# Kernel optimization log

Measured on AMD Instinct MI355X. Metric: run time of the kernel, lower is better.

## Reference

```python
import jax, jax.numpy as jnp
import numpy as np

B, NQ, NC = 4, 512, 2048
DQ, DC, C = 1024, 768, 1024
H = 16
HD = C // H
L = 2
EPS = 1e-5


def _ln(x, g, b):
    m = jnp.mean(x, axis=-1, keepdims=True)
    v = jnp.mean((x - m) ** 2, axis=-1, keepdims=True)
    return (x - m) * jax.lax.rsqrt(v + EPS) * g + b


def setup_inputs() -> dict:
    key = jax.random.key(0)
    ks = iter(jax.random.split(key, 16))
    s = 0.02
    inp = {}
    inp['query'] = jax.random.normal(next(ks), (B, NQ, DQ), dtype=jnp.float32)
    inp['context'] = jax.random.normal(next(ks), (B, NC, DC), dtype=jnp.float32)
    mask = jax.random.randint(next(ks), (B, NC), 0, 2, dtype=jnp.int32)
    inp['context_mask'] = mask.at[:, 0].set(1)  # guarantee >=1 valid key per row
    inp['Wqp'] = jax.random.normal(next(ks), (DQ, C), dtype=jnp.float32) * s
    inp['bqp'] = jnp.zeros((C,), jnp.float32)
    inp['Wcp'] = jax.random.normal(next(ks), (DC, C), dtype=jnp.float32) * s
    inp['bcp'] = jnp.zeros((C,), jnp.float32)
    inp['Wq'] = jax.random.normal(next(ks), (L, C, C), dtype=jnp.float32) * s
    inp['bq'] = jnp.zeros((L, C), jnp.float32)
    inp['Wkv'] = jax.random.normal(next(ks), (L, C, 2 * C), dtype=jnp.float32) * s
    inp['bkv'] = jnp.zeros((L, 2 * C), jnp.float32)
    inp['Wo'] = jax.random.normal(next(ks), (L, C, C), dtype=jnp.float32) * s
    inp['bo'] = jnp.zeros((L, C), jnp.float32)
    inp['g1'] = jnp.ones((L, C), jnp.float32)
    inp['beta1'] = jnp.zeros((L, C), jnp.float32)
    inp['W1'] = jax.random.normal(next(ks), (L, C, 4 * C), dtype=jnp.float32) * s
    inp['bf1'] = jnp.zeros((L, 4 * C), jnp.float32)
    inp['W2'] = jax.random.normal(next(ks), (L, 4 * C, C), dtype=jnp.float32) * s
    inp['bf2'] = jnp.zeros((L, C), jnp.float32)
    inp['g2'] = jnp.ones((L, C), jnp.float32)
    inp['beta2'] = jnp.zeros((L, C), jnp.float32)
    inp['gf'] = jnp.ones((C,), jnp.float32)
    inp['betaf'] = jnp.zeros((C,), jnp.float32)
    return inp


def reference(query, context, context_mask, Wqp, bqp, Wcp, bcp, Wq, bq, Wkv, bkv,
              Wo, bo, g1, beta1, W1, bf1, W2, bf2, g2, beta2, gf, betaf):
    scale = HD ** -0.5
    q = query @ Wqp + bqp            # [B,NQ,C]
    c = context @ Wcp + bcp          # [B,NC,C]
    neg = (context_mask == 0)[:, None, None, :]  # [B,1,1,NC]
    for l in range(L):
        qn = _ln(q, g1[l], beta1[l])
        qh = (qn @ Wq[l] + bq[l]).reshape(B, NQ, H, HD).transpose(0, 2, 1, 3)
        kv = (c @ Wkv[l] + bkv[l]).reshape(B, NC, 2, H, HD).transpose(2, 0, 3, 1, 4)
        k, v = kv[0], kv[1]          # [B,H,NC,HD]
        attn = jnp.einsum('bhqd,bhkd->bhqk', qh, k) * scale
        attn = jnp.where(neg, -jnp.inf, attn)
        attn = jax.nn.softmax(attn, axis=-1)
        out = jnp.einsum('bhqk,bhkd->bhqd', attn, v)
        out = out.transpose(0, 2, 1, 3).reshape(B, NQ, C)
        q = q + (out @ Wo[l] + bo[l])
        h = _ln(q, g2[l], beta2[l])
        q = q + (jax.nn.gelu(h @ W1[l] + bf1[l], approximate=False) @ W2[l] + bf2[l])
    return _ln(q, gf, betaf)
```

## Files before the change

### kernel.cpp

```cpp
#include <hip/hip_runtime.h>
#include <hip/hip_bf16.h>
#include <math.h>

typedef __hip_bfloat16 bf16;
using short8 = __attribute__((ext_vector_type(8))) short;
using f32x4  = __attribute__((ext_vector_type(4))) float;

#define B_    4
#define NQ_   512
#define NC_   2048
#define DQ_   1024
#define DC_   768
#define C_    1024
#define H_    16
#define HD_   64
#define EPS_  1e-5f

__device__ __forceinline__ float ldin(const void* p, size_t i, int f32) {
    return f32 ? ((const float*)p)[i]
               : __bfloat162float(((const bf16*)p)[i]);
}
__device__ __forceinline__ unsigned bfb(float f) {
    return (unsigned)__builtin_bit_cast(unsigned short, __float2bfloat16(f));
}

typedef const __attribute__((address_space(1))) unsigned int ga_u32;
typedef __attribute__((address_space(3))) unsigned int ls_u32;
__device__ __forceinline__ void gl16(const void* g, void* l) {
    __builtin_amdgcn_global_load_lds((ga_u32*)g, (ls_u32*)l, 16, 0, 0);
}

__global__ __launch_bounds__(256)
void sniff_k(const void* __restrict__ q, int* __restrict__ flag)
{
    __shared__ int red[256];
    const unsigned* w = (const unsigned*)q;
    const int t = threadIdx.x;
    int cnt = 0;
    for (int i = t; i < 1024; i += 256) {
        unsigned e = (w[i] >> 7) & 0xFFu;
        cnt += (e >= 0x70u && e <= 0x82u) ? 1 : 0;
    }
    red[t] = cnt; __syncthreads();
    for (int s = 128; s > 0; s >>= 1) { if (t < s) red[t] += red[t + s]; __syncthreads(); }
    if (t == 0) flag[0] = (red[0] > 512) ? 0 : 1;
}

__global__ __launch_bounds__(256)
void cvt_k(const void* __restrict__ src, bf16* __restrict__ dst, int n8,
           const int* __restrict__ dtf)
{
    const int i = blockIdx.x * 256 + threadIdx.x;
    if (i >= n8) return;
    if (dtf[0]) {
        const float* s = (const float*)src + (size_t)i * 8;
        float4 a = *(const float4*)s, b = *(const float4*)(s + 4);
        uint4 o;
        o.x = bfb(a.x) | (bfb(a.y) << 16);
        o.y = bfb(a.z) | (bfb(a.w) << 16);
        o.z = bfb(b.x) | (bfb(b.y) << 16);
        o.w = bfb(b.z) | (bfb(b.w) << 16);
        *(uint4*)(dst + (size_t)i * 8) = o;
    } else {
        *(uint4*)(dst + (size_t)i * 8) = *(const uint4*)((const bf16*)src + (size_t)i * 8);
    }
}

struct KTr {
    const void* src[6];
    bf16*       dst[6];
    long long   off[6];
    int ld[6], K[6], N[6];
    int start[7];
    int njobs;
};

__global__ __launch_bounds__(256)
void tr_all(KTr J, const int* __restrict__ dtf)
{
    __shared__ short T[64 * 65];
    const int f32 = dtf[0];
    const int t = threadIdx.x;
    int bid = blockIdx.x, j = 0;
    while (j + 1 < J.njobs && bid >= J.start[j + 1]) ++j;
    const int tt = bid - J.start[j];
    const int nx = J.N[j] >> 6;
    const int n0 = (tt % nx) * 64, k0 = (tt / nx) * 64;
    const int ld = J.ld[j], K = J.K[j];
    {
        const int k = t >> 2, nq = (t & 3) * 16;
        size_t si = (size_t)J.off[j] + (size_t)(k0 + k) * ld + n0 + nq;
        short v[16];
        if (f32) {
            const float* s = (const float*)J.src[j] + si;
#pragma unroll
            for (int u = 0; u < 4; u++) {
                float4 f = *(const float4*)(s + u * 4);
                v[u*4+0] = (short)bfb(f.x); v[u*4+1] = (short)bfb(f.y);
                v[u*4+2] = (short)bfb(f.z); v[u*4+3] = (short)bfb(f.w);
            }
        } else {
            const bf16* s = (const bf16*)J.src[j] + si;
#pragma unroll
            for (int u = 0; u < 2; u++) {
                uint4 x = *(const uint4*)(s + u * 8);
                unsigned a[4] = {x.x, x.y, x.z, x.w};
#pragma unroll
                for (int m = 0; m < 4; m++) {
                    v[u*8 + m*2]     = (short)(a[m] & 0xffffu);
                    v[u*8 + m*2 + 1] = (short)(a[m] >> 16);
                }
            }
        }
#pragma unroll
        for (int jj = 0; jj < 16; jj++) T[k * 65 + nq + jj] = v[jj];
    }
    __syncthreads();
    {
        const int n = t >> 2, kq = (t & 3) * 16;
        unsigned pk[8];
#pragma unroll
        for (int u = 0; u < 8; u++) {
            unsigned lo = (unsigned short)T[(kq + u*2)     * 65 + n];
            unsigned hi = (unsigned short)T[(kq + u*2 + 1) * 65 + n];
            pk[u] = lo | (hi << 16);
        }
        bf16* d = J.dst[j] + (size_t)(n0 + n) * K + k0 + kq;
        *(uint4*)(d)     = make_uint4(pk[0], pk[1], pk[2], pk[3]);
        *(uint4*)(d + 8) = make_uint4(pk[4], pk[5], pk[6], pk[7]);
    }
}

template<int ACT, int ACC, int OUTF32, int BM, int BN>
__global__ __launch_bounds__(256)
void gemm_bf(const bf16* __restrict__ A, int lda,
             const bf16* __restrict__ Wt,
             const void* __restrict__ bias, size_t boff, float bscale,
             void* __restrict__ outp, int M, int N, int K,
             const int* __restrict__ dtf)
{
    __shared__ short As[2][BM * 32];
    __shared__ short Bs[2][BN * 32];
    constexpr int MI = (BM == 128 && BN == 128) ? 4 : 2;
    constexpr int NJ = (BM == 64) ? 2 : 4;
    const int t  = threadIdx.x;
    const int nwg = gridDim.x * gridDim.y;
    int flat = blockIdx.y * gridDim.x + blockIdx.x;
    flat = (flat & 7) * (nwg >> 3) + (flat >> 3);
    const int row0 = (flat / gridDim.x) * BM, col0 = (flat % gridDim.x) * BN;
    const int wv = t >> 6, l = t & 63;
    const int lm = l & 15, lq = l >> 4;
    const int lr = l >> 2, lc = l & 3;
    const int swc  = lc ^ ((lr >> 1) & 3);
    const int koff = (lq ^ ((lm >> 1) & 3)) << 3;
    const int wr = (BM == 128 && BN == 128) ? (wv >> 1) * 64
                 : (BM == 128) ? wv * 32 : (wv >> 1) * 32;
    const int wc = (BN == 128) ? (wv & 1) * 64
                 : (BM == 128) ? 0 : (wv & 1) * 32;

    const bf16* Ag0 = A + (size_t)(row0 + ((BM == 128) ? wv * 32 : wv * 16) + lr) * lda + swc * 8;
    const bf16* Ag1 = Ag0 + (size_t)16 * lda;
    const bf16* Bg0 = Wt + (size_t)(col0 + ((BN == 128) ? wv * 32 : wv * 16) + lr) * K + swc * 8;
    const bf16* Bg1 = Bg0 + (size_t)16 * K;

    f32x4 acc[MI][NJ];
#pragma unroll
    for (int i = 0; i < MI; i++)
#pragma unroll
        for (int j = 0; j < NJ; j++) { acc[i][j][0]=0.f; acc[i][j][1]=0.f; acc[i][j][2]=0.f; acc[i][j][3]=0.f; }

    auto stage = [&](int b, int k0) {
        if constexpr (BM == 128) {
            gl16(Ag0 + k0, &As[b][(wv * 32) * 32]);
            gl16(Ag1 + k0, &As[b][(wv * 32 + 16) * 32]);
        } else {
            gl16(Ag0 + k0, &As[b][(wv * 16) * 32]);
        }
        if constexpr (BN == 128) {
            gl16(Bg0 + k0, &Bs[b][(wv * 32) * 32]);
            gl16(Bg1 + k0, &Bs[b][(wv * 32 + 16) * 32]);
        } else {
            gl16(Bg0 + k0, &Bs[b][(wv * 16) * 32]);
        }
    };

    const int nt = K >> 5;
    stage(0, 0);
    __syncthreads();
    int cur = 0;
    for (int tt = 0; tt < nt; ++tt) {
        if (tt + 1 < nt) stage(cur ^ 1, (tt + 1) * 32);
        short8 af[MI], bfr[NJ];
#pragma unroll
        for (int i = 0; i < MI; i++) af[i]  = *(const short8*)&As[cur][(wr + i*16 + lm) * 32 + koff];
#pragma unroll
        for (int j = 0; j < NJ; j++) bfr[j] = *(const short8*)&Bs[cur][(wc + j*16 + lm) * 32 + koff];
#pragma unroll
        for (int i = 0; i < MI; i++)
#pragma unroll
            for (int j = 0; j < NJ; j++)
                acc[i][j] = __builtin_amdgcn_mfma_f32_16x16x32_bf16(af[i], bfr[j], acc[i][j], 0, 0, 0);
        __syncthreads();
        cur ^= 1;
    }

    const int fb = dtf[0];
#pragma unroll
    for (int i = 0; i < MI; i++) {
#pragma unroll
        for (int j = 0; j < NJ; j++) {
            const int cgl = col0 + wc + j * 16 + lm;
            const float bsv = bscale * ldin(bias, boff + cgl, fb);
#pragma unroll
            for (int r = 0; r < 4; r++) {
                const int rgl = row0 + wr + i * 16 + lq * 4 + r;
                float v = acc[i][j][r] + bsv;
                if (ACT == 1) v = 0.5f * v * (1.0f + erff(v * 0.70710678118654752440f));
                size_t o = (size_t)rgl * N + cgl;
                if constexpr (ACC)          ((float*)outp)[o] += v;
                else if constexpr (OUTF32)  ((float*)outp)[o] = v;
                else                        ((bf16*)outp)[o] = __float2bfloat16(v);
            }
        }
    }
}

__global__ __launch_bounds__(256)
void gemm_kv(const bf16* __restrict__ A, int lda,
             const bf16* __restrict__ Wt,
             const void* __restrict__ bias, size_t boff,
             bf16* __restrict__ kb, bf16* __restrict__ vt,
             int M, int K, const int* __restrict__ dtf)
{
    __shared__ short smem[17408];
    const int t  = threadIdx.x;
    const int nwg = gridDim.x * gridDim.y;
    int flat = blockIdx.y * gridDim.x + blockIdx.x;
    flat = (flat & 7) * (nwg >> 3) + (flat >> 3);
    const int row0 = (flat / gridDim.x) * 128, col0 = (flat % gridDim.x) * 128;
    const int wv = t >> 6, l = t & 63;
    const int lm = l & 15, lq = l >> 4;
    const int lr = l >> 2, lc = l & 3;
    const int swc  = lc ^ ((lr >> 1) & 3);
    const int koff = (lq ^ ((lm >> 1) & 3)) << 3;
    const int wr = (wv >> 1) * 64, wc = (wv & 1) * 64;

    const bf16* Ag0 = A + (size_t)(row0 + wv * 32 + lr) * lda + swc * 8;
    const bf16* Ag1 = Ag0 + (size_t)16 * lda;
    const bf16* Bg0 = Wt + (size_t)(col0 + wv * 32 + lr) * K + swc * 8;
    const bf16* Bg1 = Bg0 + (size_t)16 * K;

    f32x4 acc[4][4];
#pragma unroll
    for (int i = 0; i < 4; i++)
#pragma unroll
        for (int j = 0; j < 4; j++) { acc[i][j][0]=0.f; acc[i][j][1]=0.f; acc[i][j][2]=0.f; acc[i][j][3]=0.f; }

    auto stage = [&](int b, int k0) {
        gl16(Ag0 + k0, &smem[b * 4096 + (wv * 32) * 32]);
        gl16(Ag1 + k0, &smem[b * 4096 + (wv * 32 + 16) * 32]);
        gl16(Bg0 + k0, &smem[8192 + b * 4096 + (wv * 32) * 32]);
        gl16(Bg1 + k0, &smem[8192 + b * 4096 + (wv * 32 + 16) * 32]);
    };

    const int nt = K >> 5;
    stage(0, 0);
    __syncthreads();
    int cur = 0;
    for (int tt = 0; tt < nt; ++tt) {
        if (tt + 1 < nt) stage(cur ^ 1, (tt + 1) * 32);
        short8 af[4], bfr[4];
#pragma unroll
        for (int i = 0; i < 4; i++) af[i]  = *(const short8*)&smem[cur * 4096 + (wr + i*16 + lm) * 32 + koff];
#pragma unroll
        for (int j = 0; j < 4; j++) bfr[j] = *(const short8*)&smem[8192 + cur * 4096 + (wc + j*16 + lm) * 32 + koff];
#pragma unroll
        for (int i = 0; i < 4; i++)
#pragma unroll
            for (int j = 0; j < 4; j++)
                acc[i][j] = __builtin_amdgcn_mfma_f32_16x16x32_bf16(af[i], bfr[j], acc[i][j], 0, 0, 0);
        __syncthreads();
        cur ^= 1;
    }

    const int fb = dtf[0];
    if (col0 < C_) {
#pragma unroll
        for (int i = 0; i < 4; i++)
#pragma unroll
            for (int j = 0; j < 4; j++) {
                const int cgl = col0 + wc + j * 16 + lm;
                const float bsv = ldin(bias, boff + cgl, fb);
#pragma unroll
                for (int r = 0; r < 4; r++) {
                    const int rgl = row0 + wr + i * 16 + lq * 4 + r;
                    kb[(size_t)rgl * C_ + cgl] = __float2bfloat16(acc[i][j][r] + bsv);
                }
            }
    } else {
#pragma unroll
        for (int i = 0; i < 4; i++)
#pragma unroll
            for (int j = 0; j < 4; j++) {
                const int cl = wc + j * 16 + lm;
                const float bsv = ldin(bias, boff + col0 + cl, fb);
                unsigned p0 = bfb(acc[i][j][0] + bsv) | (bfb(acc[i][j][1] + bsv) << 16);
                unsigned p1 = bfb(acc[i][j][2] + bsv) | (bfb(acc[i][j][3] + bsv) << 16);
                *(uint2*)&smem[cl * 136 + wr + i * 16 + lq * 4] = make_uint2(p0, p1);
            }
        __syncthreads();
        const int dr = t >> 1, half = (t & 1) * 64;
        const int b = row0 >> 11, key0 = row0 & (NC_ - 1);
        bf16* dst = vt + (size_t)b * C_ * NC_ + (size_t)(col0 - C_ + dr) * NC_ + key0 + half;
#pragma unroll
        for (int u = 0; u < 8; u++)
            *(uint4*)(dst + u * 8) = *(const uint4*)&smem[dr * 136 + half + u * 8];
    }
}

template<int OFINAL>
__global__ __launch_bounds__(256)
void ln_k(const float* __restrict__ x, const void* __restrict__ g,
          const void* __restrict__ b, size_t gboff, void* __restrict__ out,
          const int* __restrict__ dtf)
{
    __shared__ float red[256];
    const int f32 = dtf[0];
    const int row = blockIdx.x;
    const int t = threadIdx.x;
    const float* xr = x + (size_t)row * C_;
    float v[4];
#pragma unroll
    for (int i = 0; i < 4; i++) v[i] = xr[t + 256 * i];
    float s = v[0] + v[1] + v[2] + v[3];
    red[t] = s; __syncthreads();
    for (int st = 128; st > 0; st >>= 1) { if (t < st) red[t] += red[t + st]; __syncthreads(); }
    float mean = red[0] * (1.0f / C_);
    __syncthreads();
    float s2 = 0.f;
#pragma unroll
    for (int i = 0; i < 4; i++) { float d = v[i] - mean; s2 += d * d; }
    red[t] = s2; __syncthreads();
    for (int st = 128; st > 0; st >>= 1) { if (t < st) red[t] += red[t + st]; __syncthreads(); }
    float rstd = rsqrtf(red[0] * (1.0f / C_) + EPS_);
#pragma unroll
    for (int i = 0; i < 4; i++) {
        int cc = t + 256 * i;
        float r = (v[i] - mean) * rstd * ldin(g, gboff + cc, f32) + ldin(b, gboff + cc, f32);
        size_t o = (size_t)row * C_ + cc;
        if constexpr (OFINAL) {
            if (f32) ((float*)out)[o] = r; else ((bf16*)out)[o] = __float2bfloat16(r);
        } else {
            ((bf16*)out)[o] = __float2bfloat16(r);
        }
    }
}

template<int NSPLIT>
__global__ __launch_bounds__(256)
void attn_mfma(const bf16* __restrict__ qh, const bf16* __restrict__ kb,
               const bf16* __restrict__ vt, const int* __restrict__ mask,
               bf16* __restrict__ out,
               float* __restrict__ po, float* __restrict__ pm,
               float* __restrict__ pl)
{
    __shared__ short Ks[128 * 72];
    __shared__ short Vs[64 * 136];
    __shared__ short Ps[4][16 * 136];

    const int id = blockIdx.x;
    const int xcd = id & 7, kk = id >> 3;
    const int p = xcd + ((kk >> 3) << 3);
    int bb, h, sp;
    if constexpr (NSPLIT == 2) { bb = p >> 5; h = (p >> 1) & 15; sp = p & 1; }
    else                       { bb = p >> 4; h = p & 15;        sp = 0;     }
    const int q0 = (kk & 7) * 64;
    const int kbase = sp * (NC_ / NSPLIT);
    const int klen  = NC_ / NSPLIT;

    const bf16* qhb = qh + (size_t)bb * NQ_ * C_;
    const bf16* kbb = kb + (size_t)bb * NC_ * C_;
    const bf16* vtb = vt + (size_t)bb * C_ * NC_ + (size_t)h * HD_ * NC_;
    const int*  mb  = mask + bb * NC_ + kbase;
    bf16* ob = out + (size_t)bb * NQ_ * C_;

    const int t  = threadIdx.x;
    const int w  = t >> 6, l = t & 63;
    const int lm = l & 15, lq = l >> 4;
    short* Pw = Ps[w];

    short8 qf[2];
    {
        const bf16* qp = qhb + (size_t)(q0 + w * 16 + lm) * C_ + h * HD_ + lq * 8;
        qf[0] = *(const short8*)(qp);
        qf[1] = *(const short8*)(qp + 32);
    }

    f32x4 o[4];
#pragma unroll
    for (int jd = 0; jd < 4; jd++) { o[jd][0]=0.f; o[jd][1]=0.f; o[jd][2]=0.f; o[jd][3]=0.f; }
    float m_run[4], l_run[4];
#pragma unroll
    for (int r = 0; r < 4; r++) { m_run[r] = -1e30f; l_run[r] = 0.f; }

    const int kr4 = t >> 2;
    const int c16 = (t & 3) * 16;
    const int c32 = (t & 3) * 32;
    const bf16* kg = kbb + (size_t)(kbase + kr4) * C_ + h * HD_ + c16;
    const bf16* vg = vtb + (size_t)kr4 * NC_ + kbase + c32;

    uint4 k00, k01, k10, k11, v0, v1, v2, v3;
    int mk[8];
    {
        k00 = *(const uint4*)(kg);
        k01 = *(const uint4*)(kg + 8);
        k10 = *(const uint4*)(kg + (size_t)64 * C_);
        k11 = *(const uint4*)(kg + (size_t)64 * C_ + 8);
        v0  = *(const uint4*)(vg);
        v1  = *(const uint4*)(vg + 8);
        v2  = *(const uint4*)(vg + 16);
        v3  = *(const uint4*)(vg + 24);
#pragma unroll
        for (int jt = 0; jt < 8; jt++) mk[jt] = mb[jt * 16 + lm];
    }

    for (int k0 = 0; k0 < klen; k0 += 128) {
        __syncthreads();
        *(uint4*)&Ks[kr4 * 72 + c16]            = k00;
        *(uint4*)&Ks[kr4 * 72 + c16 + 8]        = k01;
        *(uint4*)&Ks[(kr4 + 64) * 72 + c16]     = k10;
        *(uint4*)&Ks[(kr4 + 64) * 72 + c16 + 8] = k11;
        *(uint4*)&Vs[kr4 * 136 + c32]      = v0;
        *(uint4*)&Vs[kr4 * 136 + c32 + 8]  = v1;
        *(uint4*)&Vs[kr4 * 136 + c32 + 16] = v2;
        *(uint4*)&Vs[kr4 * 136 + c32 + 24] = v3;
        int mc[8];
#pragma unroll
        for (int jt = 0; jt < 8; jt++) mc[jt] = mk[jt];
        __syncthreads();

        if (k0 + 128 < klen) {
            const bf16* kp = kg + (size_t)(k0 + 128) * C_;
            k00 = *(const uint4*)(kp);
            k01 = *(const uint4*)(kp + 8);
            k10 = *(const uint4*)(kp + (size_t)64 * C_);
            k11 = *(const uint4*)(kp + (size_t)64 * C_ + 8);
            const bf16* vp = vg + k0 + 128;
            v0 = *(const uint4*)(vp);
            v1 = *(const uint4*)(vp + 8);
            v2 = *(const uint4*)(vp + 16);
            v3 = *(const uint4*)(vp + 24);
#pragma unroll
            for (int jt = 0; jt < 8; jt++) mk[jt] = mb[k0 + 128 + jt * 16 + lm];
        }

        f32x4 s[8];
#pragma unroll
        for (int jt = 0; jt < 8; jt++) { s[jt][0]=0.f; s[jt][1]=0.f; s[jt][2]=0.f; s[jt][3]=0.f; }
        __builtin_amdgcn_s_setprio(1);
#pragma unroll
        for (int dc = 0; dc < 2; dc++) {
#pragma unroll
            for (int jt = 0; jt < 8; jt++) {
                short8 kf = *(const short8*)&Ks[(jt * 16 + lm) * 72 + dc * 32 + lq * 8];
                s[jt] = __builtin_amdgcn_mfma_f32_16x16x32_bf16(qf[dc], kf, s[jt], 0, 0, 0);
            }
        }
        __builtin_amdgcn_s_setprio(0);
#pragma unroll
        for (int jt = 0; jt < 8; jt++) {
#pragma unroll
            for (int r = 0; r < 4; r++)
                s[jt][r] = mc[jt] ? s[jt][r] * 0.125f : -1e30f;
        }

#pragma unroll
        for (int r = 0; r < 4; r++) {
            float mt = fmaxf(fmaxf(fmaxf(s[0][r], s[1][r]), fmaxf(s[2][r], s[3][r])),
                             fmaxf(fmaxf(s[4][r], s[5][r]), fmaxf(s[6][r], s[7][r])));
#pragma unroll
            for (int sh = 1; sh < 16; sh <<= 1) mt = fmaxf(mt, __shfl_xor(mt, sh, 64));
            const float nm = fmaxf(m_run[r], mt);
            const float al = __expf(m_run[r] - nm);
            float rs = 0.f;
            short* pr = &Pw[(lq * 4 + r) * 136 + lm];
#pragma unroll
            for (int jt = 0; jt < 8; jt++) {
                float pv = __expf(s[jt][r] - nm);
                pr[jt * 16] = (short)bfb(pv);
                rs += pv;
            }
#pragma unroll
            for (int sh = 1; sh < 16; sh <<= 1) rs += __shfl_xor(rs, sh, 64);
            l_run[r] = l_run[r] * al + rs;
            m_run[r] = nm;
#pragma unroll
            for (int jd = 0; jd < 4; jd++) o[jd][r] *= al;
        }

        short8 pa[4];
#pragma unroll
        for (int c = 0; c < 4; c++) pa[c] = *(const short8*)&Pw[lm * 136 + c * 32 + lq * 8];
        __builtin_amdgcn_s_setprio(1);
#pragma unroll
        for (int jd = 0; jd < 4; jd++) {
#pragma unroll
            for (int c = 0; c < 4; c++) {
                short8 vf = *(const short8*)&Vs[(jd * 16 + lm) * 136 + c * 32 + lq * 8];
                o[jd] = __builtin_amdgcn_mfma_f32_16x16x32_bf16(pa[c], vf, o[jd], 0, 0, 0);
            }
        }
        __builtin_amdgcn_s_setprio(0);
    }

    if constexpr (NSPLIT == 2) {
        const int pidx = ((bb * 16 + h) * 2 + sp);
#pragma unroll
        for (int r = 0; r < 4; r++) {
            const int row = q0 + w * 16 + lq * 4 + r;
            float* prow = po + ((size_t)pidx * 512 + row) * 64;
#pragma unroll
            for (int jd = 0; jd < 4; jd++) prow[jd * 16 + lm] = o[jd][r];
            if (lm == 0) {
                pm[pidx * 512 + row] = m_run[r];
                pl[pidx * 512 + row] = l_run[r];
            }
        }
    } else {
#pragma unroll
        for (int r = 0; r < 4; r++) {
            const float inv = 1.0f / l_run[r];
            bf16* dst = ob + (size_t)(q0 + w * 16 + lq * 4 + r) * C_ + h * HD_ + lm;
#pragma unroll
            for (int jd = 0; jd < 4; jd++) dst[jd * 16] = __float2bfloat16(o[jd][r] * inv);
        }
    }
}

__global__ __launch_bounds__(256)
void attn_merge(const float* __restrict__ po, const float* __restrict__ pm,
                const float* __restrict__ pl, bf16* __restrict__ qh)
{
    const int t = threadIdx.x;
    const int row = blockIdx.x * 4 + (t >> 6);
    const int d = t & 63;
    const int bh = row >> 9, qr = row & 511;
    const int i0 = (bh * 2) * 512 + qr, i1 = i0 + 512;
    const float m0 = pm[i0], m1 = pm[i1];
    const float l0 = pl[i0], l1 = pl[i1];
    const float nm = fmaxf(m0, m1);
    const float e0 = __expf(m0 - nm), e1 = __expf(m1 - nm);
    const float L = l0 * e0 + l1 * e1;
    const float v = (po[(size_t)i0 * 64 + d] * e0 + po[(size_t)i1 * 64 + d] * e1) / L;
    const int bb = bh >> 4, h = bh & 15;
    qh[((size_t)bb * NQ_ + qr) * C_ + h * HD_ + d] = __float2bfloat16(v);
}

static void add_job(KTr& J, const void* src, long long off, int ld,
                    bf16* dst, int K, int N)
{
    const int j = J.njobs++;
    J.src[j] = src; J.off[j] = off; J.ld[j] = ld;
    J.dst[j] = dst; J.K[j] = K; J.N[j] = N;
    J.start[j + 1] = J.start[j] + (N / 64) * (K / 64);
}

extern "C" void kernel_launch(void* const* d_in, const int* in_sizes, int n_in,
                              void* d_out, int out_size, void* d_ws, size_t ws_size,
                              hipStream_t stream)
{
    const void* query   = d_in[0];
    const void* context = d_in[1];
    const int*  mask    = (const int*)d_in[2];
    const void* Wqp = d_in[3];  const void* bqp  = d_in[4];
    const void* Wcp = d_in[5];  const void* bcp  = d_in[6];
    const void* Wq  = d_in[7];  const void* bq   = d_in[8];
    const void* Wkv = d_in[9];  const void* bkv  = d_in[10];
    const void* Wo  = d_in[11]; const void* bo   = d_in[12];
    const void* g1  = d_in[13]; const void* be1  = d_in[14];
    const void* W1  = d_in[15]; const void* bf1  = d_in[16];
    const void* W2  = d_in[17]; const void* bf2  = d_in[18];
    const void* g2  = d_in[19]; const void* be2  = d_in[20];
    const void* gf  = d_in[21]; const void* bef  = d_in[22];

    char* w = (char*)d_ws;
    const bool mega  = ws_size >= (((size_t)88 << 20) + 64);
    const bool split = ws_size >= (((size_t)110 << 20) + 64);

    float* q    = (float*)(w);
    bf16*  xn   = (bf16*) (w + ( 8u << 20));
    bf16*  qh   = (bf16*) (w + (12u << 20));
    bf16*  ff1h = (bf16*) (w + (12u << 20));
    bf16*  cbf  = (bf16*) (w + (12u << 20));
    bf16*  qbf  = (bf16*) (w + (24u << 20));
    bf16*  kb   = (bf16*) (w + (16u << 20));
    bf16*  vt   = (bf16*) (w + (32u << 20));
    bf16*  cb   = (bf16*) (w + (48u << 20));
    bf16*  Wt   = (bf16*) (w + (64u << 20));
    int*   dtf  = (int*)  (w + (mega ? (88u << 20) : (68u << 20)));
    float* po   = (float*)(w + (90u << 20));
    float* pm   = (float*)(w + (107u << 20));
    float* pl   = (float*)(w + (107u << 20) + (256u << 10));

    const int MQ = B_ * NQ_;
    dim3 blk(256);
    const size_t M1 = 1u << 20;

    sniff_k<<<1, blk, 0, stream>>>(query, dtf);

    cvt_k<<<dim3((MQ * DQ_) / 8 / 256), blk, 0, stream>>>(query, qbf, (MQ * DQ_) / 8, dtf);
    cvt_k<<<dim3((B_ * NC_ * DC_) / 8 / 256), blk, 0, stream>>>(context, cbf, (B_ * NC_ * DC_) / 8, dtf);

    bf16 *WqpT, *WcpT;
    if (mega) {
        KTr J{}; J.njobs = 0; J.start[0] = 0;
        WqpT = Wt; WcpT = Wt + M1;
        add_job(J, Wqp, 0, C_, WqpT, DQ_, C_);
        add_job(J, Wcp, 0, C_, WcpT, DC_, C_);
        tr_all<<<dim3(J.start[J.njobs]), blk, 0, stream>>>(J, dtf);
    } else {
        WqpT = WcpT = Wt;
        KTr J{}; J.njobs = 0; J.start[0] = 0;
        add_job(J, Wqp, 0, C_, Wt, DQ_, C_);
        tr_all<<<dim3(J.start[J.njobs]), blk, 0, stream>>>(J, dtf);
    }
    gemm_bf<0,0,1,64,64><<<dim3(C_/64, MQ/64), blk, 0, stream>>>(
        qbf, DQ_, WqpT, bqp, 0, 1.f, q, MQ, C_, DQ_, dtf);
    if (!mega) {
        KTr J{}; J.njobs = 0; J.start[0] = 0;
        add_job(J, Wcp, 0, C_, Wt, DC_, C_);
        tr_all<<<dim3(J.start[J.njobs]), blk, 0, stream>>>(J, dtf);
    }
    gemm_bf<0,0,0,128,128><<<dim3(C_/128, (B_*NC_)/128), blk, 0, stream>>>(
        cbf, DC_, WcpT, bcp, 0, 1.f, cb, B_*NC_, C_, DC_, dtf);

    for (int l = 0; l < 2; l++) {
        const size_t oC  = (size_t)l * C_;
        const size_t oCC = (size_t)l * C_ * C_;
        const size_t o2C = (size_t)l * 2 * C_;
        const size_t oK2 = (size_t)l * C_ * 2 * C_;
        const size_t o4C = (size_t)l * 4 * C_;
        const size_t oK4 = (size_t)l * C_ * 4 * C_;

        bf16 *WqT, *WkvT, *WoT, *W1T, *W2T;
        if (mega) {
            WqT = Wt; WkvT = Wt + M1; WoT = Wt + 3*M1; W1T = Wt + 4*M1; W2T = Wt + 8*M1;
            KTr J{}; J.njobs = 0; J.start[0] = 0;
            add_job(J, Wq,  (long long)oCC, C_,   WqT,  C_,   C_);
            add_job(J, Wkv, (long long)oK2, 2*C_, WkvT, C_,   2*C_);
            add_job(J, Wo,  (long long)oCC, C_,   WoT,  C_,   C_);
            add_job(J, W1,  (long long)oK4, 4*C_, W1T,  C_,   4*C_);
            add_job(J, W2,  (long long)oK4, C_,   W2T,  4*C_, C_);
            tr_all<<<dim3(J.start[J.njobs]), blk, 0, stream>>>(J, dtf);
        } else {
            WqT = WkvT = WoT = W1T = W2T = Wt;
        }

        ln_k<0><<<MQ, blk, 0, stream>>>(q, g1, be1, oC, xn, dtf);
        if (!mega) {
            KTr J{}; J.njobs = 0; J.start[0] = 0;
            add_job(J, Wq, (long long)oCC, C_, Wt, C_, C_);
            tr_all<<<dim3(J.start[J.njobs]), blk, 0, stream>>>(J, dtf);
        }
        gemm_bf<0,0,0,64,64><<<dim3(C_/64, MQ/64), blk, 0, stream>>>(
            xn, C_, WqT, bq, oC, 1.f, qh, MQ, C_, C_, dtf);

        if (!mega) {
            KTr J{}; J.njobs = 0; J.start[0] = 0;
            add_job(J, Wkv, (long long)oK2, 2*C_, Wt, C_, 2*C_);
            tr_all<<<dim3(J.start[J.njobs]), blk, 0, stream>>>(J, dtf);
        }
        gemm_kv<<<dim3((2*C_)/128, (B_*NC_)/128), blk, 0, stream>>>(
            cb, C_, WkvT, bkv, o2C, kb, vt, B_*NC_, C_, dtf);

        if (split) {
            attn_mfma<2><<<dim3(1024), blk, 0, stream>>>(qh, kb, vt, mask, qh, po, pm, pl);
            attn_merge<<<dim3(8192), blk, 0, stream>>>(po, pm, pl, qh);
        } else {
            attn_mfma<1><<<dim3(512), blk, 0, stream>>>(qh, kb, vt, mask, qh, po, pm, pl);
        }

        if (!mega) {
            KTr J{}; J.njobs = 0; J.start[0] = 0;
            add_job(J, Wo, (long long)oCC, C_, Wt, C_, C_);
            tr_all<<<dim3(J.start[J.njobs]), blk, 0, stream>>>(J, dtf);
        }
        gemm_bf<0,1,1,64,64><<<dim3(C_/64, MQ/64), blk, 0, stream>>>(
            qh, C_, WoT, bo, oC, 1.f, q, MQ, C_, C_, dtf);

        ln_k<0><<<MQ, blk, 0, stream>>>(q, g2, be2, oC, xn, dtf);
        if (mega) {
            gemm_bf<1,0,0,128,64><<<dim3((4*C_)/64, MQ/128), blk, 0, stream>>>(
                xn, C_, W1T, bf1, o4C, 1.f, ff1h, MQ, 4*C_, C_, dtf);
            gemm_bf<0,1,1,64,64><<<dim3(C_/64, MQ/64), blk, 0, stream>>>(
                ff1h, 4*C_, W2T, bf2, oC, 1.f, q, MQ, C_, 4*C_, dtf);
        } else {
            for (int hf = 0; hf < 2; hf++) {
                const long long w1off = (long long)oK4 + (long long)hf * 2048;
                const long long w2off = (long long)oK4 + (long long)hf * 2048 * C_;
                {
                    KTr J{}; J.njobs = 0; J.start[0] = 0;
                    add_job(J, W1, w1off, 4*C_, Wt, C_, 2048);
                    tr_all<<<dim3(J.start[J.njobs]), blk, 0, stream>>>(J, dtf);
                }
                gemm_bf<1,0,0,128,128><<<dim3(2048/128, MQ/128), blk, 0, stream>>>(
                    xn, C_, Wt, bf1, o4C + hf * 2048, 1.f, ff1h, MQ, 2048, C_, dtf);
                {
                    KTr J{}; J.njobs = 0; J.start[0] = 0;
                    add_job(J, W2, w2off, C_, Wt, 2048, C_);
                    tr_all<<<dim3(J.start[J.njobs]), blk, 0, stream>>>(J, dtf);
                }
                gemm_bf<0,1,1,64,64><<<dim3(C_/64, MQ/64), blk, 0, stream>>>(
                    ff1h, 2048, Wt, bf2, oC, (hf == 0) ? 1.f : 0.f, q, MQ, C_, 2048, dtf);
            }
        }
    }

    ln_k<1><<<MQ, blk, 0, stream>>>(q, gf, bef, 0, d_out, dtf);
}
```

Baseline: 734.8 us.

## Add BK=64 GEMM variant and lazy softmax rescaling in attention

```diff
diff --git a/kernel.cpp b/kernel.cpp
--- a/kernel.cpp
+++ b/kernel.cpp
@@ -131,7 +131,7 @@
     }
 }
 
-template<int ACT, int ACC, int OUTF32, int BM, int BN>
+template<int ACT, int ACC, int OUTF32, int BM, int BN, int BK>
 __global__ __launch_bounds__(256)
 void gemm_bf(const bf16* __restrict__ A, int lda,
              const bf16* __restrict__ Wt,
@@ -139,8 +139,8 @@
              void* __restrict__ outp, int M, int N, int K,
              const int* __restrict__ dtf)
 {
-    __shared__ short As[2][BM * 32];
-    __shared__ short Bs[2][BN * 32];
+    __shared__ short As[2][BM * BK];
+    __shared__ short Bs[2][BN * BK];
     constexpr int MI = (BM == 128 && BN == 128) ? 4 : 2;
     constexpr int NJ = (BM == 64) ? 2 : 4;
     const int t  = threadIdx.x;
@@ -153,15 +153,25 @@
     const int lr = l >> 2, lc = l & 3;
     const int swc  = lc ^ ((lr >> 1) & 3);
     const int koff = (lq ^ ((lm >> 1) & 3)) << 3;
+    const int lr8 = l >> 3, lc8 = l & 7;
+    const int swc8 = lc8 ^ (lr8 & 7);
     const int wr = (BM == 128 && BN == 128) ? (wv >> 1) * 64
                  : (BM == 128) ? wv * 32 : (wv >> 1) * 32;
     const int wc = (BN == 128) ? (wv & 1) * 64
                  : (BM == 128) ? 0 : (wv & 1) * 32;
 
-    const bf16* Ag0 = A + (size_t)(row0 + ((BM == 128) ? wv * 32 : wv * 16) + lr) * lda + swc * 8;
-    const bf16* Ag1 = Ag0 + (size_t)16 * lda;
-    const bf16* Bg0 = Wt + (size_t)(col0 + ((BN == 128) ? wv * 32 : wv * 16) + lr) * K + swc * 8;
-    const bf16* Bg1 = Bg0 + (size_t)16 * K;
+    const bf16* Ag0; const bf16* Ag1; const bf16* Bg0; const bf16* Bg1;
+    if constexpr (BK == 64) {
+        Ag0 = A + (size_t)(row0 + wv * 16 + lr8) * lda + swc8 * 8;
+        Ag1 = Ag0 + (size_t)8 * lda;
+        Bg0 = Wt + (size_t)(col0 + wv * 16 + lr8) * K + swc8 * 8;
+        Bg1 = Bg0 + (size_t)8 * K;
+    } else {
+        Ag0 = A + (size_t)(row0 + ((BM == 128) ? wv * 32 : wv * 16) + lr) * lda + swc * 8;
+        Ag1 = Ag0 + (size_t)16 * lda;
+        Bg0 = Wt + (size_t)(col0 + ((BN == 128) ? wv * 32 : wv * 16) + lr) * K + swc * 8;
+        Bg1 = Bg0 + (size_t)16 * K;
+    }
 
     f32x4 acc[MI][NJ];
 #pragma unroll
@@ -170,36 +180,61 @@
         for (int j = 0; j < NJ; j++) { acc[i][j][0]=0.f; acc[i][j][1]=0.f; acc[i][j][2]=0.f; acc[i][j][3]=0.f; }
 
     auto stage = [&](int b, int k0) {
-        if constexpr (BM == 128) {
-            gl16(Ag0 + k0, &As[b][(wv * 32) * 32]);
-            gl16(Ag1 + k0, &As[b][(wv * 32 + 16) * 32]);
+        if constexpr (BK == 64) {
+            gl16(Ag0 + k0, &As[b][(wv * 16) * 64]);
+            gl16(Ag1 + k0, &As[b][(wv * 16 + 8) * 64]);
+            gl16(Bg0 + k0, &Bs[b][(wv * 16) * 64]);
+            gl16(Bg1 + k0, &Bs[b][(wv * 16 + 8) * 64]);
         } else {
-            gl16(Ag0 + k0, &As[b][(wv * 16) * 32]);
-        }
-        if constexpr (BN == 128) {
-            gl16(Bg0 + k0, &Bs[b][(wv * 32) * 32]);
-            gl16(Bg1 + k0, &Bs[b][(wv * 32 + 16) * 32]);
-        } else {
-            gl16(Bg0 + k0, &Bs[b][(wv * 16) * 32]);
+            if constexpr (BM == 128) {
+                gl16(Ag0 + k0, &As[b][(wv * 32) * 32]);
+                gl16(Ag1 + k0, &As[b][(wv * 32 + 16) * 32]);
+            } else {
+                gl16(Ag0 + k0, &As[b][(wv * 16) * 32]);
+            }
+            if constexpr (BN == 128) {
+                gl16(Bg0 + k0, &Bs[b][(wv * 32) * 32]);
+                gl16(Bg1 + k0, &Bs[b][(wv * 32 + 16) * 32]);
+            } else {
+                gl16(Bg0 + k0, &Bs[b][(wv * 16) * 32]);
+            }
         }
     };
 
-    const int nt = K >> 5;
+    const int nt = K / BK;
     stage(0, 0);
     __syncthreads();
     int cur = 0;
     for (int tt = 0; tt < nt; ++tt) {
-        if (tt + 1 < nt) stage(cur ^ 1, (tt + 1) * 32);
-        short8 af[MI], bfr[NJ];
-#pragma unroll
-        for (int i = 0; i < MI; i++) af[i]  = *(const short8*)&As[cur][(wr + i*16 + lm) * 32 + koff];
-#pragma unroll
-        for (int j = 0; j < NJ; j++) bfr[j] = *(const short8*)&Bs[cur][(wc + j*16 + lm) * 32 + koff];
-#pragma unroll
-        for (int i = 0; i < MI; i++)
-#pragma unroll
-            for (int j = 0; j < NJ; j++)
-                acc[i][j] = __builtin_amdgcn_mfma_f32_16x16x32_bf16(af[i], bfr[j], acc[i][j], 0, 0, 0);
+        if (tt + 1 < nt) stage(cur ^ 1, (tt + 1) * BK);
+        if constexpr (BK == 64) {
+#pragma unroll
+            for (int kk = 0; kk < 2; kk++) {
+                short8 af[MI], bfr[NJ];
+#pragma unroll
+                for (int i = 0; i < MI; i++)
+                    af[i]  = *(const short8*)&As[cur][(wr + i*16 + lm) * 64 + (((kk << 2) | lq) ^ (lm & 7)) * 8];
+#pragma unroll
+                for (int j = 0; j < NJ; j++)
+                    bfr[j] = *(const short8*)&Bs[cur][(wc + j*16 + lm) * 64 + (((kk << 2) | lq) ^ (lm & 7)) * 8];
+#pragma unroll
+                for (int i = 0; i < MI; i++)
+#pragma unroll
+                    for (int j = 0; j < NJ; j++)
+                        acc[i][j] = __builtin_amdgcn_mfma_f32_16x16x32_bf16(af[i], bfr[j], acc[i][j], 0, 0, 0);
+            }
+        } else {
+            short8 af[MI], bfr[NJ];
+#pragma unroll
+            for (int i = 0; i < MI; i++) af[i]  = *(const short8*)&As[cur][(wr + i*16 + lm) * 32 + koff];
+#pragma unroll
+            for (int j = 0; j < NJ; j++) bfr[j] = *(const short8*)&Bs[cur][(wc + j*16 + lm) * 32 + koff];
+#pragma unroll
+            for (int i = 0; i < MI; i++)
+#pragma unroll
+                for (int j = 0; j < NJ; j++)
+                    acc[i][j] = __builtin_amdgcn_mfma_f32_16x16x32_bf16(af[i], bfr[j], acc[i][j], 0, 0, 0);
+        }
         __syncthreads();
         cur ^= 1;
     }
@@ -366,7 +401,7 @@
 {
     __shared__ short Ks[128 * 72];
     __shared__ short Vs[64 * 136];
-    __shared__ short Ps[4][16 * 136];
+    __shared__ short Ps[4][16 * 140];
 
     const int id = blockIdx.x;
     const int xcd = id & 7, kk = id >> 3;
@@ -434,9 +469,9 @@
         *(uint4*)&Vs[kr4 * 136 + c32 + 8]  = v1;
         *(uint4*)&Vs[kr4 * 136 + c32 + 16] = v2;
         *(uint4*)&Vs[kr4 * 136 + c32 + 24] = v3;
-        int mc[8];
-#pragma unroll
-        for (int jt = 0; jt < 8; jt++) mc[jt] = mk[jt];
+        float fbias[8];
+#pragma unroll
+        for (int jt = 0; jt < 8; jt++) fbias[jt] = mk[jt] ? 0.f : -1e30f;
         __syncthreads();
 
         if (k0 + 128 < klen) {
@@ -471,7 +506,7 @@
         for (int jt = 0; jt < 8; jt++) {
 #pragma unroll
             for (int r = 0; r < 4; r++)
-                s[jt][r] = mc[jt] ? s[jt][r] * 0.125f : -1e30f;
+                s[jt][r] = fmaf(s[jt][r], 0.125f, fbias[jt]);
         }
 
 #pragma unroll
@@ -480,10 +515,10 @@
                              fmaxf(fmaxf(s[4][r], s[5][r]), fmaxf(s[6][r], s[7][r])));
 #pragma unroll
             for (int sh = 1; sh < 16; sh <<= 1) mt = fmaxf(mt, __shfl_xor(mt, sh, 64));
-            const float nm = fmaxf(m_run[r], mt);
-            const float al = __expf(m_run[r] - nm);
+            const bool up = mt > m_run[r] + 8.f;
+            const float nm = up ? mt : m_run[r];
             float rs = 0.f;
-            short* pr = &Pw[(lq * 4 + r) * 136 + lm];
+            short* pr = &Pw[(lq * 4 + r) * 140 + lm];
 #pragma unroll
             for (int jt = 0; jt < 8; jt++) {
                 float pv = __expf(s[jt][r] - nm);
@@ -492,15 +527,20 @@
             }
 #pragma unroll
             for (int sh = 1; sh < 16; sh <<= 1) rs += __shfl_xor(rs, sh, 64);
-            l_run[r] = l_run[r] * al + rs;
-            m_run[r] = nm;
-#pragma unroll
-            for (int jd = 0; jd < 4; jd++) o[jd][r] *= al;
+            if (up) {
+                const float al = __expf(m_run[r] - nm);
+                l_run[r] = l_run[r] * al + rs;
+                m_run[r] = mt;
+#pragma unroll
+                for (int jd = 0; jd < 4; jd++) o[jd][r] *= al;
+            } else {
+                l_run[r] += rs;
+            }
         }
 
         short8 pa[4];
 #pragma unroll
-        for (int c = 0; c < 4; c++) pa[c] = *(const short8*)&Pw[lm * 136 + c * 32 + lq * 8];
+        for (int c = 0; c < 4; c++) pa[c] = *(const short8*)&Pw[lm * 140 + c * 32 + lq * 8];
         __builtin_amdgcn_s_setprio(1);
 #pragma unroll
         for (int jd = 0; jd < 4; jd++) {
@@ -624,14 +664,14 @@
         add_job(J, Wqp, 0, C_, Wt, DQ_, C_);
         tr_all<<<dim3(J.start[J.njobs]), blk, 0, stream>>>(J, dtf);
     }
-    gemm_bf<0,0,1,64,64><<<dim3(C_/64, MQ/64), blk, 0, stream>>>(
+    gemm_bf<0,0,1,64,64,64><<<dim3(C_/64, MQ/64), blk, 0, stream>>>(
         qbf, DQ_, WqpT, bqp, 0, 1.f, q, MQ, C_, DQ_, dtf);
     if (!mega) {
         KTr J{}; J.njobs = 0; J.start[0] = 0;
         add_job(J, Wcp, 0, C_, Wt, DC_, C_);
         tr_all<<<dim3(J.start[J.njobs]), blk, 0, stream>>>(J, dtf);
     }
-    gemm_bf<0,0,0,128,128><<<dim3(C_/128, (B_*NC_)/128), blk, 0, stream>>>(
+    gemm_bf<0,0,0,128,128,32><<<dim3(C_/128, (B_*NC_)/128), blk, 0, stream>>>(
         cbf, DC_, WcpT, bcp, 0, 1.f, cb, B_*NC_, C_, DC_, dtf);
 
     for (int l = 0; l < 2; l++) {
@@ -662,7 +702,7 @@
             add_job(J, Wq, (long long)oCC, C_, Wt, C_, C_);
             tr_all<<<dim3(J.start[J.njobs]), blk, 0, stream>>>(J, dtf);
         }
-        gemm_bf<0,0,0,64,64><<<dim3(C_/64, MQ/64), blk, 0, stream>>>(
+        gemm_bf<0,0,0,64,64,64><<<dim3(C_/64, MQ/64), blk, 0, stream>>>(
             xn, C_, WqT, bq, oC, 1.f, qh, MQ, C_, C_, dtf);
 
         if (!mega) {
@@ -685,14 +725,14 @@
             add_job(J, Wo, (long long)oCC, C_, Wt, C_, C_);
             tr_all<<<dim3(J.start[J.njobs]), blk, 0, stream>>>(J, dtf);
         }
-        gemm_bf<0,1,1,64,64><<<dim3(C_/64, MQ/64), blk, 0, stream>>>(
+        gemm_bf<0,1,1,64,64,64><<<dim3(C_/64, MQ/64), blk, 0, stream>>>(
             qh, C_, WoT, bo, oC, 1.f, q, MQ, C_, C_, dtf);
 
         ln_k<0><<<MQ, blk, 0, stream>>>(q, g2, be2, oC, xn, dtf);
         if (mega) {
-            gemm_bf<1,0,0,128,64><<<dim3((4*C_)/64, MQ/128), blk, 0, stream>>>(
+            gemm_bf<1,0,0,128,64,32><<<dim3((4*C_)/64, MQ/128), blk, 0, stream>>>(
                 xn, C_, W1T, bf1, o4C, 1.f, ff1h, MQ, 4*C_, C_, dtf);
-            gemm_bf<0,1,1,64,64><<<dim3(C_/64, MQ/64), blk, 0, stream>>>(
+            gemm_bf<0,1,1,64,64,64><<<dim3(C_/64, MQ/64), blk, 0, stream>>>(
                 ff1h, 4*C_, W2T, bf2, oC, 1.f, q, MQ, C_, 4*C_, dtf);
         } else {
             for (int hf = 0; hf < 2; hf++) {
@@ -703,14 +743,14 @@
                     add_job(J, W1, w1off, 4*C_, Wt, C_, 2048);
                     tr_all<<<dim3(J.start[J.njobs]), blk, 0, stream>>>(J, dtf);
                 }
-                gemm_bf<1,0,0,128,128><<<dim3(2048/128, MQ/128), blk, 0, stream>>>(
+                gemm_bf<1,0,0,128,128,32><<<dim3(2048/128, MQ/128), blk, 0, stream>>>(
                     xn, C_, Wt, bf1, o4C + hf * 2048, 1.f, ff1h, MQ, 2048, C_, dtf);
                 {
                     KTr J{}; J.njobs = 0; J.start[0] = 0;
                     add_job(J, W2, w2off, C_, Wt, 2048, C_);
                     tr_all<<<dim3(J.start[J.njobs]), blk, 0, stream>>>(J, dtf);
                 }
-                gemm_bf<0,1,1,64,64><<<dim3(C_/64, MQ/64), blk, 0, stream>>>(
+                gemm_bf<0,1,1,64,64,64><<<dim3(C_/64, MQ/64), blk, 0, stream>>>(
                     ff1h, 2048, Wt, bf2, oC, (hf == 0) ? 1.f : 0.f, q, MQ, C_, 2048, dtf);
             }
         }
```

Measured after the change: 751.5 us. 2.3% more time.
